# Performance work log

Hardware: AMD Instinct MI355X
Metric: run time of the kernel (lower is better)

## Reference

```python
import jax, jax.numpy as jnp
import numpy as np

RSD = 9   # robot_state_dim
HSD = 5   # human_state_dim (human feature slice width = HSD+1 = 6)
XD = 32   # X_dim
NEG = -9e15


def _lin(x, w, b):
    return x @ w + b


def _gat(X, adj, w0, b0, w1, b1):
    # X: [B,N,F]; pairwise concat feature (i,j) = [X_i, X_j] -> [B,N,N,2F]
    B, N, F = X.shape
    Xi = jnp.broadcast_to(X[:, :, None, :], (B, N, N, F))
    Xj = jnp.broadcast_to(X[:, None, :, :], (B, N, N, F))
    pair = jnp.concatenate([Xi, Xj], axis=-1)              # [B,N,N,2F]
    h = jax.nn.relu(_lin(pair, w0, b0))                    # [B,N,N,2F]
    A = _lin(h, w1, b1)[..., 0]                            # [B,N,N]
    e = jnp.where(A > 0, A, 0.04 * A)                      # LeakyReLU(0.04)
    att = jax.nn.softmax(jnp.where(adj > 0, e, NEG), axis=2)
    return jnp.einsum('bij,bjf->bif', att, X)


def setup_inputs() -> dict:
    key = jax.random.key(0)
    ks = jax.random.split(key, 32)
    s = 0.05
    d = {
        'state': jax.random.normal(ks[0], (512, 50, 15), jnp.float32),
        'dropout': 0,
        # w_r: Linear(9,64) ReLU Linear(64,32) ReLU
        'wr_w0': jax.random.normal(ks[1], (RSD, 64)) * s, 'wr_b0': jnp.zeros((64,)),
        'wr_w1': jax.random.normal(ks[2], (64, XD)) * s, 'wr_b1': jnp.zeros((XD,)),
        # w_h: Linear(6,64) ReLU Linear(64,32) ReLU
        'wh_w0': jax.random.normal(ks[3], (HSD + 1, 64)) * s, 'wh_b0': jnp.zeros((64,)),
        'wh_w1': jax.random.normal(ks[4], (64, XD)) * s, 'wh_b1': jnp.zeros((XD,)),
        # gat0 w_a: Linear(64,64) ReLU Linear(64,1)
        'g0_w0': jax.random.normal(ks[5], (2 * XD, 2 * XD)) * s, 'g0_b0': jnp.zeros((2 * XD,)),
        'g0_w1': jax.random.normal(ks[6], (2 * XD, 1)) * s, 'g0_b1': jnp.zeros((1,)),
        # gat1 w_a
        'g1_w0': jax.random.normal(ks[7], (2 * XD, 2 * XD)) * s, 'g1_b0': jnp.zeros((2 * XD,)),
        'g1_w1': jax.random.normal(ks[8], (2 * XD, 1)) * s, 'g1_b1': jnp.zeros((1,)),
        # value_net: Linear(32,150) ReLU Linear(150,100) ReLU Linear(100,1) ReLU
        'v_w0': jax.random.normal(ks[9], (XD, 150)) * s, 'v_b0': jnp.zeros((150,)),
        'v_w1': jax.random.normal(ks[10], (150, 100)) * s, 'v_b1': jnp.zeros((100,)),
        'v_w2': jax.random.normal(ks[11], (100, 1)) * s, 'v_b2': jnp.zeros((1,)),
    }
    return d


def reference(state, dropout, wr_w0, wr_b0, wr_w1, wr_b1, wh_w0, wh_b0, wh_w1, wh_b1,
              g0_w0, g0_b0, g0_w1, g0_b1, g1_w0, g1_b0, g1_w1, g1_b1,
              v_w0, v_b0, v_w1, v_b1, v_w2, v_b2):
    B, N, _ = state.shape
    robot = state[:, 0, :RSD]                               # [B,9]
    humans = state[:, :, RSD:]                              # [B,N,6]
    r_emb = jax.nn.relu(_lin(jax.nn.relu(_lin(robot, wr_w0, wr_b0)), wr_w1, wr_b1))[:, None, :]
    h_emb = jax.nn.relu(_lin(jax.nn.relu(_lin(humans, wh_w0, wh_b0)), wh_w1, wh_b1))
    X = jnp.concatenate([r_emb, h_emb], axis=1)             # [B,N+1,32]
    Num = N + 1
    adj = jnp.ones((Num, Num), state.dtype).at[1:, 0].set(0.0)
    adj = jnp.broadcast_to(adj[None], (B, Num, Num))
    H1 = _gat(X, adj, g0_w0, g0_b0, g0_w1, g0_b1)
    H2 = _gat(H1, adj, g1_w0, g1_b0, g1_w1, g1_b1)
    output = H1 + H2 + X                                    # skip_connection=True
    o = output[:, 0, :]
    o = jax.nn.relu(_lin(o, v_w0, v_b0))
    o = jax.nn.relu(_lin(o, v_w1, v_b1))
    o = jax.nn.relu(_lin(o, v_w2, v_b2))                    # last_relu=True
    return o
```

## Files before the change

kernel.cpp:

```cpp
#include <hip/hip_runtime.h>
#include <hip/hip_bf16.h>


typedef float f4 __attribute__((ext_vector_type(4)));
typedef const float* cfp;

__device__ __forceinline__ f4 fma4(float s, f4 v, f4 a) { return a + s * v; }
__device__ __forceinline__ f4 max4(f4 a, f4 b) {
  f4 r;
#pragma unroll
  for (int i = 0; i < 4; ++i) r[i] = fmaxf(a[i], b[i]);
  return r;
}

#define NN 51
#define HID 64
#define XD 32
#define XS 9
#define ES 52

__global__ __launch_bounds__(512, 4)
void value_net_kernel(cfp state,
                      cfp wr_w0, cfp wr_b0, cfp wr_w1, cfp wr_b1,
                      cfp wh_w0, cfp wh_b0, cfp wh_w1, cfp wh_b1,
                      cfp g0_w0, cfp g0_b0, cfp g0_w1, cfp g0_b1,
                      cfp g1_w0, cfp g1_b0, cfp g1_w1, cfp g1_b1,
                      cfp v_w0, cfp v_b0, cfp v_w1, cfp v_b1,
                      cfp v_w2, cfp v_b2,
                      float* out)
{
  __shared__ f4 sX4[52 * XS];
  __shared__ f4 sH14[52 * XS];
  __shared__ f4 sU4[52 * 17];
  __shared__ f4 sV4[52 * 17];
  __shared__ f4 sWE4[1024];
  __shared__ f4 sB04[16];
  __shared__ f4 sW14[16];
  __shared__ float sRH[64];
  __shared__ float sO[32];
  __shared__ float sM1[152];
  __shared__ float sM2[104];

  float* sX  = (float*)sX4;
  float* sH1 = (float*)sH14;
  float* sE  = (float*)sWE4;
  float* sHH = (float*)sU4;
  const f4* sWh4 = (const f4*)sV4;

  const int tid = threadIdx.x;
  const int b = blockIdx.x;
  cfp st = state + b * 750;

  const float gb0 = g0_b1[0];
  const float gb1 = g1_b1[0];

  {
    const f4* g0w04 = (const f4*)g0_w0;
    for (int i = tid; i < 1024; i += 512) sWE4[i] = g0w04[i];
    const f4* whw14 = (const f4*)wh_w1;
    f4* sWh4w = (f4*)sV4;
    if (tid < 512) sWh4w[tid] = whw14[tid];
  }
  if (tid < HID) {
    ((float*)sB04)[tid] = g0_b0[tid];
    ((float*)sW14)[tid] = g0_w1[tid];
    float a = wr_b0[tid];
#pragma unroll
    for (int k = 0; k < 9; ++k) a = fmaf(st[k], wr_w0[k * HID + tid], a);
    sRH[tid] = fmaxf(a, 0.f);
  }
  if (tid >= 64 && tid < 64 + XS) sX4[51 * XS + (tid - 64)] = (f4){0,0,0,0};
  for (int idx = tid; idx < 50 * HID; idx += 512) {
    int i = idx >> 6, t = idx & 63;
    cfp hp = st + i * 15 + 9;
    float a = wh_b0[t];
#pragma unroll
    for (int k = 0; k < 6; ++k) a = fmaf(hp[k], wh_w0[k * HID + t], a);
    sHH[i * 68 + t] = fmaxf(a, 0.f);
  }
  __syncthreads();

  if (tid < 200) {
    int ip = tid >> 3, fg = tid & 7;
    f4 a0 = { wh_b1[fg * 4 + 0], wh_b1[fg * 4 + 1],
              wh_b1[fg * 4 + 2], wh_b1[fg * 4 + 3] };
    f4 a1 = a0;
    const f4* h0 = sU4 + ip * 17;
    const f4* h1 = sU4 + (ip + 25) * 17;
#pragma unroll 4
    for (int tg = 0; tg < 16; ++tg) {
      f4 ha = h0[tg], hb = h1[tg];
#pragma unroll
      for (int e = 0; e < 4; ++e) {
        f4 w = sWh4[(tg * 4 + e) * 8 + fg];
        a0 = fma4(ha[e], w, a0);
        a1 = fma4(hb[e], w, a1);
      }
    }
    f4 z = {0,0,0,0};
    sX4[(1 + ip) * XS + fg] = max4(a0, z);
    sX4[(26 + ip) * XS + fg] = max4(a1, z);
  } else if (tid >= 448 && tid < 448 + XD) {
    int t = tid - 448;
    float a = wr_b1[t];
#pragma unroll 8
    for (int k = 0; k < HID; ++k) a = fmaf(sRH[k], wr_w1[k * XD + t], a);
    sX[t] = fmaxf(a, 0.f);
  }
  __syncthreads();

  if (tid < 272) {
    int ip = tid >> 4, tg = tid & 15;
    f4 au[3] = {{0,0,0,0},{0,0,0,0},{0,0,0,0}};
    f4 av[3] = {{0,0,0,0},{0,0,0,0},{0,0,0,0}};
#pragma unroll 2
    for (int kg = 0; kg < 8; ++kg) {
      f4 x0 = sX4[ip * XS + kg];
      f4 x1 = sX4[(ip + 17) * XS + kg];
      f4 x2 = sX4[(ip + 34) * XS + kg];
#pragma unroll
      for (int e = 0; e < 4; ++e) {
        int k = kg * 4 + e;
        f4 wU = sWE4[k * 16 + tg];
        f4 wV = sWE4[(k + 32) * 16 + tg];
        au[0] = fma4(x0[e], wU, au[0]); av[0] = fma4(x0[e], wV, av[0]);
        au[1] = fma4(x1[e], wU, au[1]); av[1] = fma4(x1[e], wV, av[1]);
        au[2] = fma4(x2[e], wU, au[2]); av[2] = fma4(x2[e], wV, av[2]);
      }
    }
    f4 b0v = sB04[tg];
#pragma unroll
    for (int r = 0; r < 3; ++r) {
      int row = ip + 17 * r;
      sU4[row * 17 + tg] = au[r] + b0v;
      sV4[row * 17 + tg] = av[r];
    }
  }
  __syncthreads();

  if (tid < 289) {
    int it = tid / 17, jt = tid - (tid / 17) * 17;
    const f4* U0 = sU4 + it * 17;
    const f4* V0 = sV4 + jt * 17;
    f4 acc[3][3] = {};
    const f4 z = {0,0,0,0};
#pragma unroll 4
    for (int g = 0; g < 16; ++g) {
      f4 uu[3] = {U0[g], U0[289 + g], U0[578 + g]};
      f4 vv[3] = {V0[g], V0[289 + g], V0[578 + g]};
      f4 w = sW14[g];
#pragma unroll
      for (int r = 0; r < 3; ++r)
#pragma unroll
        for (int cc = 0; cc < 3; ++cc)
          acc[r][cc] += max4(uu[r] + vv[cc], z) * w;
    }
#pragma unroll
    for (int r = 0; r < 3; ++r) {
      int i = it + 17 * r;
#pragma unroll
      for (int cc = 0; cc < 3; ++cc) {
        int j = jt + 17 * cc;
        f4 A4 = acc[r][cc];
        float A = (A4[0] + A4[1]) + (A4[2] + A4[3]) + gb0;
        float e = A > 0.f ? A : 0.04f * A;
        sE[i * ES + j] = (j == 0 && i > 0) ? -1e30f : e;
      }
    }
  }
  __syncthreads();

  {
    int lane = tid & 63, w = tid >> 6;
    for (int r = w; r < NN; r += 8) {
      float* row = sE + r * ES;
      float e = (lane < NN) ? row[lane] : -3.0e38f;
      float m = e;
#pragma unroll
      for (int o = 32; o; o >>= 1) m = fmaxf(m, __shfl_xor(m, o, 64));
      float p = (lane < NN) ? __expf(e - m) : 0.f;
      float s = p;
#pragma unroll
      for (int o = 32; o; o >>= 1) s += __shfl_xor(s, o, 64);
      if (lane < NN) row[lane] = p / s;
      else if (lane == NN) row[lane] = 0.f;
    }
  }
  __syncthreads();

  if (tid < 208) {
    int ip = tid >> 3, q = tid & 7;
    const f4* a0 = (const f4*)(sE + ip * ES);
    const f4* a1 = (const f4*)(sE + (ip + 26) * ES);
    f4 b0 = {0,0,0,0}, b1 = {0,0,0,0};
    for (int jg = 0; jg < 13; ++jg) {
      f4 t0 = a0[jg], t1 = a1[jg];
#pragma unroll
      for (int e = 0; e < 4; ++e) {
        f4 x = sX4[(jg * 4 + e) * XS + q];
        b0 = fma4(t0[e], x, b0);
        b1 = fma4(t1[e], x, b1);
      }
    }
    sH14[ip * XS + q] = b0;
    sH14[(ip + 26) * XS + q] = b1;
  } else if (tid >= 384) {
    int t = tid - 384;
    const f4* g1w = (const f4*)g1_w0;
#pragma unroll
    for (int i = 0; i < 4; ++i) sU4[t + 128 * i] = g1w[512 + t + 128 * i];
  } else if (tid >= 352 && tid < 368) {
    sB04[tid - 352] = ((const f4*)g1_b0)[tid - 352];
  } else if (tid >= 368 && tid < 384) {
    sW14[tid - 368] = ((const f4*)g1_w1)[tid - 368];
  }
  __syncthreads();

  if (tid < 272) {
    int jp = tid >> 4, tg = tid & 15;
    f4 av[3] = {{0,0,0,0},{0,0,0,0},{0,0,0,0}};
#pragma unroll 2
    for (int kg = 0; kg < 8; ++kg) {
      f4 h0 = sH14[jp * XS + kg];
      f4 h1 = sH14[(jp + 17) * XS + kg];
      f4 h2 = sH14[(jp + 34) * XS + kg];
#pragma unroll
      for (int e = 0; e < 4; ++e) {
        f4 wV = sU4[(kg * 4 + e) * 16 + tg];
        av[0] = fma4(h0[e], wV, av[0]);
        av[1] = fma4(h1[e], wV, av[1]);
        av[2] = fma4(h2[e], wV, av[2]);
      }
    }
#pragma unroll
    for (int r = 0; r < 3; ++r) sV4[(jp + 17 * r) * 17 + tg] = av[r];
  } else if (tid < 288) {
    int tg = tid - 272;
    const f4* w0g = (const f4*)g1_w0;
    f4 au = {0,0,0,0};
#pragma unroll 2
    for (int kg = 0; kg < 8; ++kg) {
      f4 h = sH14[kg];
#pragma unroll
      for (int e = 0; e < 4; ++e) au = fma4(h[e], w0g[(kg * 4 + e) * 16 + tg], au);
    }
    sU4[512 + tg] = au + sB04[tg];
  }
  __syncthreads();

  if (tid < 64) {
    int j = tid;
    float e = -3.0e38f;
    if (j < NN) {
      f4 acc4 = {0,0,0,0};
#pragma unroll 4
      for (int g = 0; g < 16; ++g) {
        f4 u = sU4[512 + g];
        f4 v = sV4[j * 17 + g];
        f4 w = sW14[g];
        f4 z = {0,0,0,0};
        acc4 += max4(u + v, z) * w;
      }
      float acc = (acc4[0] + acc4[1]) + (acc4[2] + acc4[3]) + gb1;
      e = acc > 0.f ? acc : 0.04f * acc;
    }
    float m = e;
#pragma unroll
    for (int o = 32; o; o >>= 1) m = fmaxf(m, __shfl_xor(m, o, 64));
    float p = (j < NN) ? __expf(e - m) : 0.f;
    float s = p;
#pragma unroll
    for (int o = 32; o; o >>= 1) s += __shfl_xor(s, o, 64);
    if (j < NN) sE[j] = p / s;
  }
  __syncthreads();

  if (tid < XD) {
    float a = 0.f;
    for (int j = 0; j < NN; ++j) a = fmaf(sE[j], sH1[j * 36 + tid], a);
    sO[tid] = a + sH1[tid] + sX[tid];
  }
  __syncthreads();

  if (tid < 150) {
    float a = v_b0[tid];
#pragma unroll 8
    for (int k = 0; k < 32; ++k) a = fmaf(sO[k], v_w0[k * 150 + tid], a);
    sM1[tid] = fmaxf(a, 0.f);
  }
  __syncthreads();
  if (tid < 500) {
    int kp = tid / 50, t2 = tid % 50;
    const float2* w = (const float2*)v_w1;
    float2 acc = {0.f, 0.f};
    for (int k = kp * 15; k < kp * 15 + 15; ++k) {
      float2 ww = w[k * 50 + t2];
      float xv = sM1[k];
      acc.x = fmaf(xv, ww.x, acc.x);
      acc.y = fmaf(xv, ww.y, acc.y);
    }
    ((float2*)(sE + 768 + kp * 100))[t2] = acc;
  }
  __syncthreads();
  if (tid < 100) {
    float a = v_b1[tid];
#pragma unroll
    for (int kp = 0; kp < 10; ++kp) a += sE[768 + kp * 100 + tid];
    sM2[tid] = fmaxf(a, 0.f);
  }
  __syncthreads();
  if (tid < 64) {
    float a = sM2[tid] * v_w2[tid];
    if (tid < 36) a = fmaf(sM2[tid + 64], v_w2[tid + 64], a);
#pragma unroll
    for (int o = 32; o; o >>= 1) a += __shfl_xor(a, o, 64);
    if (tid == 0) out[b] = fmaxf(a + v_b2[0], 0.f);
  }
}

extern "C" void kernel_launch(void* const* d_in, const int* in_sizes, int n_in,
                              void* d_out, int out_size, void* d_ws, size_t ws_size,
                              hipStream_t stream) {
  cfp state = (cfp)d_in[0];
  cfp wr_w0 = (cfp)d_in[2],  wr_b0 = (cfp)d_in[3];
  cfp wr_w1 = (cfp)d_in[4],  wr_b1 = (cfp)d_in[5];
  cfp wh_w0 = (cfp)d_in[6],  wh_b0 = (cfp)d_in[7];
  cfp wh_w1 = (cfp)d_in[8],  wh_b1 = (cfp)d_in[9];
  cfp g0_w0 = (cfp)d_in[10], g0_b0 = (cfp)d_in[11];
  cfp g0_w1 = (cfp)d_in[12], g0_b1 = (cfp)d_in[13];
  cfp g1_w0 = (cfp)d_in[14], g1_b0 = (cfp)d_in[15];
  cfp g1_w1 = (cfp)d_in[16], g1_b1 = (cfp)d_in[17];
  cfp v_w0  = (cfp)d_in[18], v_b0  = (cfp)d_in[19];
  cfp v_w1  = (cfp)d_in[20], v_b1  = (cfp)d_in[21];
  cfp v_w2  = (cfp)d_in[22], v_b2  = (cfp)d_in[23];
  float* out = (float*)d_out;

  const int B = in_sizes[0] / 750;
  hipLaunchKernelGGL(value_net_kernel, dim3(B), dim3(512), 0, stream,
                     state,
                     wr_w0, wr_b0, wr_w1, wr_b1,
                     wh_w0, wh_b0, wh_w1, wh_b1,
                     g0_w0, g0_b0, g0_w1, g0_b1,
                     g1_w0, g1_b0, g1_w1, g1_b1,
                     v_w0, v_b0, v_w1, v_b1, v_w2, v_b2,
                     out);
}
```

Before: 130.6 us.

## Rebalance GAT thread mapping across more threads and drop redundant barriers

Widens the U/V projection and pairwise attention stages to use more threads, with 2 rows per thread instead of 3 and a 2x4 tile of 13 columns instead of 3x3 over 17. The human embedding layer now keeps its first-layer weights in registers and loops over rows. The robot embedding moves to the high thread range, and two __syncthreads are removed by fusing the softmax with the aggregation and the hidden bias with the final reduction. The aim is better occupancy of the 512-thread block and fewer barriers, at the cost of some idle threads and boundary checks in the pairwise tile.

After: 127.8 us. 2.1% less time.

```diff
diff --git a/kernel.cpp b/kernel.cpp
--- a/kernel.cpp
+++ b/kernel.cpp
@@ -39,11 +39,12 @@
   __shared__ float sRH[64];
   __shared__ float sO[32];
   __shared__ float sM1[152];
-  __shared__ float sM2[104];
 
   float* sX  = (float*)sX4;
   float* sH1 = (float*)sH14;
   float* sE  = (float*)sWE4;
+  float* sB0 = (float*)sB04;
+  float* sW1 = (float*)sW14;
   float* sHH = (float*)sU4;
   const f4* sWh4 = (const f4*)sV4;
 
@@ -59,24 +60,31 @@
     for (int i = tid; i < 1024; i += 512) sWE4[i] = g0w04[i];
     const f4* whw14 = (const f4*)wh_w1;
     f4* sWh4w = (f4*)sV4;
-    if (tid < 512) sWh4w[tid] = whw14[tid];
-  }
-  if (tid < HID) {
-    ((float*)sB04)[tid] = g0_b0[tid];
-    ((float*)sW14)[tid] = g0_w1[tid];
-    float a = wr_b0[tid];
-#pragma unroll
-    for (int k = 0; k < 9; ++k) a = fmaf(st[k], wr_w0[k * HID + tid], a);
-    sRH[tid] = fmaxf(a, 0.f);
+    sWh4w[tid] = whw14[tid];
   }
   if (tid >= 64 && tid < 64 + XS) sX4[51 * XS + (tid - 64)] = (f4){0,0,0,0};
-  for (int idx = tid; idx < 50 * HID; idx += 512) {
-    int i = idx >> 6, t = idx & 63;
-    cfp hp = st + i * 15 + 9;
-    float a = wh_b0[t];
-#pragma unroll
-    for (int k = 0; k < 6; ++k) a = fmaf(hp[k], wh_w0[k * HID + t], a);
-    sHH[i * 68 + t] = fmaxf(a, 0.f);
+  if (tid >= 448) {
+    int t = tid - 448;
+    sB0[t] = g0_b0[t];
+    sW1[t] = g0_w1[t];
+    float a = wr_b0[t];
+#pragma unroll
+    for (int k = 0; k < 9; ++k) a = fmaf(st[k], wr_w0[k * HID + t], a);
+    sRH[t] = fmaxf(a, 0.f);
+  }
+  {
+    int t = tid & 63, g = tid >> 6;
+    float w0r[6];
+#pragma unroll
+    for (int k = 0; k < 6; ++k) w0r[k] = wh_w0[k * HID + t];
+    float bh = wh_b0[t];
+    for (int i = g; i < 50; i += 8) {
+      cfp hp = st + i * 15 + 9;
+      float a = bh;
+#pragma unroll
+      for (int k = 0; k < 6; ++k) a = fmaf(hp[k], w0r[k], a);
+      sHH[i * 68 + t] = fmaxf(a, 0.f);
+    }
   }
   __syncthreads();
 
@@ -109,62 +117,61 @@
   }
   __syncthreads();
 
-  if (tid < 272) {
+  if (tid < 416) {
     int ip = tid >> 4, tg = tid & 15;
-    f4 au[3] = {{0,0,0,0},{0,0,0,0},{0,0,0,0}};
-    f4 av[3] = {{0,0,0,0},{0,0,0,0},{0,0,0,0}};
+    f4 au0 = {0,0,0,0}, av0 = {0,0,0,0}, au1 = {0,0,0,0}, av1 = {0,0,0,0};
 #pragma unroll 2
     for (int kg = 0; kg < 8; ++kg) {
       f4 x0 = sX4[ip * XS + kg];
-      f4 x1 = sX4[(ip + 17) * XS + kg];
-      f4 x2 = sX4[(ip + 34) * XS + kg];
+      f4 x1 = sX4[(ip + 26) * XS + kg];
 #pragma unroll
       for (int e = 0; e < 4; ++e) {
         int k = kg * 4 + e;
         f4 wU = sWE4[k * 16 + tg];
         f4 wV = sWE4[(k + 32) * 16 + tg];
-        au[0] = fma4(x0[e], wU, au[0]); av[0] = fma4(x0[e], wV, av[0]);
-        au[1] = fma4(x1[e], wU, au[1]); av[1] = fma4(x1[e], wV, av[1]);
-        au[2] = fma4(x2[e], wU, au[2]); av[2] = fma4(x2[e], wV, av[2]);
+        au0 = fma4(x0[e], wU, au0); av0 = fma4(x0[e], wV, av0);
+        au1 = fma4(x1[e], wU, au1); av1 = fma4(x1[e], wV, av1);
       }
     }
     f4 b0v = sB04[tg];
-#pragma unroll
-    for (int r = 0; r < 3; ++r) {
-      int row = ip + 17 * r;
-      sU4[row * 17 + tg] = au[r] + b0v;
-      sV4[row * 17 + tg] = av[r];
-    }
-  }
-  __syncthreads();
-
-  if (tid < 289) {
-    int it = tid / 17, jt = tid - (tid / 17) * 17;
+    sU4[ip * 17 + tg] = au0 + b0v;
+    sV4[ip * 17 + tg] = av0;
+    sU4[(ip + 26) * 17 + tg] = au1 + b0v;
+    sV4[(ip + 26) * 17 + tg] = av1;
+  }
+  __syncthreads();
+
+  if (tid < 338) {
+    int it = tid / 13, jt = tid - (tid / 13) * 13;
     const f4* U0 = sU4 + it * 17;
     const f4* V0 = sV4 + jt * 17;
-    f4 acc[3][3] = {};
+    f4 acc[2][4] = {};
     const f4 z = {0,0,0,0};
 #pragma unroll 4
     for (int g = 0; g < 16; ++g) {
-      f4 uu[3] = {U0[g], U0[289 + g], U0[578 + g]};
-      f4 vv[3] = {V0[g], V0[289 + g], V0[578 + g]};
+      f4 u0 = U0[g], u1 = U0[442 + g];
+      f4 vv[4] = {V0[g], V0[221 + g], V0[442 + g], V0[663 + g]};
       f4 w = sW14[g];
 #pragma unroll
-      for (int r = 0; r < 3; ++r)
-#pragma unroll
-        for (int cc = 0; cc < 3; ++cc)
-          acc[r][cc] += max4(uu[r] + vv[cc], z) * w;
-    }
-#pragma unroll
-    for (int r = 0; r < 3; ++r) {
-      int i = it + 17 * r;
-#pragma unroll
-      for (int cc = 0; cc < 3; ++cc) {
-        int j = jt + 17 * cc;
-        f4 A4 = acc[r][cc];
-        float A = (A4[0] + A4[1]) + (A4[2] + A4[3]) + gb0;
-        float e = A > 0.f ? A : 0.04f * A;
-        sE[i * ES + j] = (j == 0 && i > 0) ? -1e30f : e;
+      for (int cc = 0; cc < 4; ++cc) {
+        acc[0][cc] += max4(u0 + vv[cc], z) * w;
+        acc[1][cc] += max4(u1 + vv[cc], z) * w;
+      }
+    }
+#pragma unroll
+    for (int r = 0; r < 2; ++r) {
+      int i = it + 26 * r;
+      if (i < NN) {
+#pragma unroll
+        for (int cc = 0; cc < 4; ++cc) {
+          int j = jt + 13 * cc;
+          if (j < NN) {
+            f4 A4 = acc[r][cc];
+            float A = (A4[0] + A4[1]) + (A4[2] + A4[3]) + gb0;
+            float e = A > 0.f ? A : 0.04f * A;
+            sE[i * ES + j] = (j == 0 && i > 0) ? -1e30f : e;
+          }
+        }
       }
     }
   }
@@ -216,26 +223,24 @@
   }
   __syncthreads();
 
-  if (tid < 272) {
+  if (tid < 416) {
     int jp = tid >> 4, tg = tid & 15;
-    f4 av[3] = {{0,0,0,0},{0,0,0,0},{0,0,0,0}};
+    f4 av0 = {0,0,0,0}, av1 = {0,0,0,0};
 #pragma unroll 2
     for (int kg = 0; kg < 8; ++kg) {
       f4 h0 = sH14[jp * XS + kg];
-      f4 h1 = sH14[(jp + 17) * XS + kg];
-      f4 h2 = sH14[(jp + 34) * XS + kg];
+      f4 h1 = sH14[(jp + 26) * XS + kg];
 #pragma unroll
       for (int e = 0; e < 4; ++e) {
         f4 wV = sU4[(kg * 4 + e) * 16 + tg];
-        av[0] = fma4(h0[e], wV, av[0]);
-        av[1] = fma4(h1[e], wV, av[1]);
-        av[2] = fma4(h2[e], wV, av[2]);
-      }
-    }
-#pragma unroll
-    for (int r = 0; r < 3; ++r) sV4[(jp + 17 * r) * 17 + tg] = av[r];
-  } else if (tid < 288) {
-    int tg = tid - 272;
+        av0 = fma4(h0[e], wV, av0);
+        av1 = fma4(h1[e], wV, av1);
+      }
+    }
+    sV4[jp * 17 + tg] = av0;
+    sV4[(jp + 26) * 17 + tg] = av1;
+  } else if (tid < 432) {
+    int tg = tid - 416;
     const f4* w0g = (const f4*)g1_w0;
     f4 au = {0,0,0,0};
 #pragma unroll 2
@@ -271,14 +276,12 @@
     float s = p;
 #pragma unroll
     for (int o = 32; o; o >>= 1) s += __shfl_xor(s, o, 64);
-    if (j < NN) sE[j] = p / s;
-  }
-  __syncthreads();
-
-  if (tid < XD) {
-    float a = 0.f;
-    for (int j = 0; j < NN; ++j) a = fmaf(sE[j], sH1[j * 36 + tid], a);
-    sO[tid] = a + sH1[tid] + sX[tid];
+    sE[j] = (j < NN) ? p / s : 0.f;
+    if (tid < XD) {
+      float a = 0.f;
+      for (int jj = 0; jj < NN; ++jj) a = fmaf(sE[jj], sH1[jj * 36 + tid], a);
+      sO[tid] = a + sH1[tid] + sX[tid];
+    }
   }
   __syncthreads();
 
@@ -289,6 +292,7 @@
     sM1[tid] = fmaxf(a, 0.f);
   }
   __syncthreads();
+
   if (tid < 500) {
     int kp = tid / 50, t2 = tid % 50;
     const float2* w = (const float2*)v_w1;
@@ -302,16 +306,18 @@
     ((float2*)(sE + 768 + kp * 100))[t2] = acc;
   }
   __syncthreads();
-  if (tid < 100) {
-    float a = v_b1[tid];
-#pragma unroll
-    for (int kp = 0; kp < 10; ++kp) a += sE[768 + kp * 100 + tid];
-    sM2[tid] = fmaxf(a, 0.f);
-  }
-  __syncthreads();
+
   if (tid < 64) {
-    float a = sM2[tid] * v_w2[tid];
-    if (tid < 36) a = fmaf(sM2[tid + 64], v_w2[tid + 64], a);
+    float a2 = v_b1[tid];
+#pragma unroll
+    for (int kp = 0; kp < 10; ++kp) a2 += sE[768 + kp * 100 + tid];
+    float a = fmaxf(a2, 0.f) * v_w2[tid];
+    if (tid < 36) {
+      float b2 = v_b1[tid + 64];
+#pragma unroll
+      for (int kp = 0; kp < 10; ++kp) b2 += sE[768 + kp * 100 + tid + 64];
+      a = fmaf(fmaxf(b2, 0.f), v_w2[tid + 64], a);
+    }
 #pragma unroll
     for (int o = 32; o; o >>= 1) a += __shfl_xor(a, o, 64);
     if (tid == 0) out[b] = fmaxf(a + v_b2[0], 0.f);
```
